# Kernel optimization log

Measured on AMD Instinct MI355X. Metric: run time of the kernel, lower is better.

The kernel has to match this reference:

```python
import jax, jax.numpy as jnp
import numpy as np

Z, H, M, N, Y = 128, 512, 256, 10, 4   # z_size, hidden, mem_vec, mem_size, y_dim
B, T = 2048, 32
SHIFT_IND = np.concatenate([np.roll(np.arange(N), s) for s in (-1, 0, 1)])  # [3*N]


def setup_inputs() -> dict:
    key = jax.random.key(0)
    ks = iter(jax.random.split(key, 48))
    def nrm(shape, s=0.05):
        return jax.random.normal(next(ks), shape, dtype=jnp.float32) * s
    d = {}
    d["z_seq"] = jax.random.normal(next(ks), (B, T, Z), dtype=jnp.float32)
    d["W_ih"] = nrm((4 * H, Z + M)); d["W_hh"] = nrm((4 * H, H))
    d["b_ih"] = jnp.zeros((4 * H,), jnp.float32); d["b_hh"] = jnp.zeros((4 * H,), jnp.float32)
    heads = {"read_key": M, "write_key": M, "erase": M, "add": M, "y": Y,
             "rks": 1, "wks": 1, "rig": 1, "wig": 1, "rsh": 3, "wsh": 3, "rshp": 1, "wshp": 1}
    for nm, o in heads.items():
        d["W_" + nm] = nrm((o, H)); d["b_" + nm] = jnp.zeros((o,), jnp.float32)
    d["memory_init"] = nrm((N, M))
    d["gamma"] = jnp.ones((Z,), jnp.float32)
    d["beta"] = jnp.zeros((Z,), jnp.float32)
    return d


def reference(z_seq, W_ih, W_hh, b_ih, b_hh,
              W_read_key, b_read_key, W_write_key, b_write_key,
              W_erase, b_erase, W_add, b_add, W_y, b_y,
              W_rks, b_rks, W_wks, b_wks, W_rig, b_rig, W_wig, b_wig,
              W_rsh, b_rsh, W_wsh, b_wsh, W_rshp, b_rshp, W_wshp, b_wshp,
              memory_init, gamma, beta):
    Bs, Ts = z_seq.shape[0], z_seq.shape[1]
    eps = 1e-8
    # context norm over the time axis (single task segment), unbiased var as torch
    mu = z_seq.mean(1, keepdims=True)
    sig = jnp.sqrt(z_seq.var(1, ddof=1, keepdims=True) + eps)
    z = (z_seq - mu) / sig * gamma + beta
    z_ext = jnp.concatenate([z, jnp.zeros((Bs, 1, Z), z.dtype)], axis=1)  # t == T step uses zero input
    shift_ind = jnp.asarray(SHIFT_IND)

    def lin(h, W, b):
        return h @ W.T + b

    def cos_sim(key_v, mem):  # key [B,M], mem [B,N,M] -> [B,N]
        dot = jnp.einsum('bm,bnm->bn', key_v, mem)
        kn = jnp.maximum(jnp.linalg.norm(key_v, axis=1, keepdims=True), eps)
        mn = jnp.maximum(jnp.linalg.norm(mem, axis=2), eps)
        return dot / (kn * mn)

    def address(key_v, strength, gate, shift_w, sharpen, w_prev, mem, use_interp):
        # content addressing (exp(s*sim)/sum == softmax), interpolation, circular shift, sharpening
        w = jax.nn.softmax(strength * cos_sim(key_v, mem), axis=1)      # [B,N]
        w = jnp.where(use_interp, gate * w + (1.0 - gate) * w_prev, w)
        w_sh = w[:, shift_ind].reshape(Bs, 3, N)                        # gather per shift
        w = jnp.einsum('bsn,bs->bn', w_sh, shift_w)
        wp = w ** sharpen
        return wp / wp.sum(1, keepdims=True)

    def step(carry, xs):
        h, c, read_vec, mem, w_read, w_write = carry
        z_t, t = xs
        lstm_in = jnp.concatenate([z_t, read_vec], axis=1)              # [B, Z+M]
        gates = lstm_in @ W_ih.T + b_ih + h @ W_hh.T + b_hh
        i, f, g, o = jnp.split(gates, 4, axis=1)
        c = jax.nn.sigmoid(f) * c + jax.nn.sigmoid(i) * jnp.tanh(g)
        h = jax.nn.sigmoid(o) * jnp.tanh(c)
        read_key = jnp.tanh(lin(h, W_read_key, b_read_key))
        write_key = jnp.tanh(lin(h, W_write_key, b_write_key))
        rks = jax.nn.softplus(lin(h, W_rks, b_rks))
        wks = jax.nn.softplus(lin(h, W_wks, b_wks))
        rig = jax.nn.sigmoid(lin(h, W_rig, b_rig))
        wig = jax.nn.sigmoid(lin(h, W_wig, b_wig))
        rsh = jax.nn.softmax(lin(h, W_rsh, b_rsh), axis=1)
        wsh = jax.nn.softmax(lin(h, W_wsh, b_wsh), axis=1)
        rshp = jax.nn.softplus(lin(h, W_rshp, b_rshp)) + 1.0
        wshp = jax.nn.softplus(lin(h, W_wshp, b_wshp)) + 1.0
        erase = jax.nn.sigmoid(lin(h, W_erase, b_erase))
        add = jnp.tanh(lin(h, W_add, b_add))
        y_lin = lin(h, W_y, b_y)
        # read (skipped at t==0; interpolation only for t>1)
        w_read_new = address(read_key, rks, rig, rsh, rshp, w_read, mem, t > 1)
        read_vec = jnp.where(t == 0, jnp.zeros((Bs, M), z_t.dtype),
                             jnp.einsum('bnm,bn->bm', mem, w_read_new))
        w_read = jnp.where(t == 0, w_read, w_read_new)
        # write (every step; interpolation only for t>0)
        w_write = address(write_key, wks, wig, wsh, wshp, w_write, mem, t > 0)
        ww = w_write[:, :, None]
        mem = mem * (1.0 - erase[:, None, :] * ww) + add[:, None, :] * ww
        return (h, c, read_vec, mem, w_read, w_write), y_lin

    carry0 = (jnp.zeros((Bs, H), z.dtype), jnp.zeros((Bs, H), z.dtype),
              jnp.zeros((Bs, M), z.dtype),
              jnp.broadcast_to(memory_init, (Bs, N, M)).astype(z.dtype),
              jnp.zeros((Bs, N), z.dtype), jnp.zeros((Bs, N), z.dtype))
    ts = jnp.arange(Ts + 1)
    _, ys = jax.lax.scan(step, carry0, (jnp.swapaxes(z_ext, 0, 1), ts))
    y_pred_linear = ys[-1]  # output of the final (t == T) step
    return y_pred_linear, jnp.argmax(y_pred_linear, axis=1)
```

## Files before the change

### kernel.cpp

```cpp
#include <hip/hip_runtime.h>
#include <hip/hip_bf16.h>

typedef __attribute__((ext_vector_type(8))) short short8;
typedef __attribute__((ext_vector_type(4))) float f32x4;

#define Bsz   2048
#define Tsz   32
#define Zsz   128
#define Hsz   512
#define Msz   256
#define Nsz   10
#define KDIM  896
#define NGATE 2048
#define NHEAD 1040
#define NHEADP 1152

#define ACT_S ((size_t)Bsz * 768)
#define ZPL_S ((size_t)33 * Bsz * 128)
#define WG_S  ((size_t)NGATE * KDIM)
#define WH_S  ((size_t)NHEADP * Hsz)

__device__ __forceinline__ float sigmoidf_(float x) { return 1.f / (1.f + expf(-x)); }
__device__ __forceinline__ float softplusf_(float x) { return x > 20.f ? x : log1pf(expf(x)); }

__device__ __forceinline__ void split3(float v, __hip_bfloat16& o1, __hip_bfloat16& o2, __hip_bfloat16& o3) {
    o1 = __float2bfloat16(v);
    float r = v - __bfloat162float(o1);
    o2 = __float2bfloat16(r);
    r -= __bfloat162float(o2);
    o3 = __float2bfloat16(r);
}

#define MFMA16(A, B, C) __builtin_amdgcn_mfma_f32_16x16x32_bf16((A), (B), (C), 0, 0, 0)

__device__ __forceinline__ void gload16(const void* g, void* l) {
    __builtin_amdgcn_global_load_lds(
        (const __attribute__((address_space(1))) void*)g,
        (__attribute__((address_space(3))) void*)l, 16, 0, 0);
}


__global__ __launch_bounds__(256) void k_lnorm(
    const float* __restrict__ z_seq, const float* __restrict__ gamma,
    const float* __restrict__ beta, __hip_bfloat16* __restrict__ zb)
{
    int idx = blockIdx.x * 256 + threadIdx.x;
    if (idx >= Bsz * Zsz) return;
    int b = idx >> 7, zi = idx & 127;
    const float* p = z_seq + (size_t)b * Tsz * Zsz + zi;
    float v[32];
    float s = 0.f;
#pragma unroll
    for (int t = 0; t < Tsz; t++) { v[t] = p[t * Zsz]; s += v[t]; }
    float mu = s * (1.f / 32.f);
    float ss = 0.f;
#pragma unroll
    for (int t = 0; t < Tsz; t++) { float d = v[t] - mu; ss += d * d; }
    float rs = rsqrtf(ss * (1.f / 31.f) + 1e-8f);
    float ga = gamma[zi], be = beta[zi];
#pragma unroll
    for (int t = 0; t <= Tsz; t++) {
        float val = (t < Tsz) ? (v[t] - mu) * rs * ga + be : 0.f;
        __hip_bfloat16 a, bq, c;
        split3(val, a, bq, c);
        size_t o = ((size_t)t * Bsz + b) * 128 + zi;
        zb[o] = a; zb[o + ZPL_S] = bq; zb[o + 2 * ZPL_S] = c;
    }
}

__global__ __launch_bounds__(256) void k_prep_wcat(
    const float* __restrict__ W_ih, const float* __restrict__ W_hh,
    const float* __restrict__ b_ih, const float* __restrict__ b_hh,
    __hip_bfloat16* __restrict__ Wt, float* __restrict__ bcat)
{
    int idx = blockIdx.x * 256 + threadIdx.x;
    if (idx >= NGATE * KDIM) return;
    int n = idx / KDIM, k = idx % KDIM;
    int jl = n & 15, g = (n >> 4) & 3, jg = n >> 6;
    int r = g * Hsz + jg * 16 + jl;
    float v = (k < 384) ? W_ih[(size_t)r * 384 + k] : W_hh[(size_t)r * Hsz + (k - 384)];
    __hip_bfloat16 a, b, c;
    split3(v, a, b, c);
    Wt[idx] = a; Wt[idx + WG_S] = b; Wt[idx + 2 * WG_S] = c;
    if (k == 0) bcat[n] = b_ih[r] + b_hh[r];
}

struct HeadP { const float* W[13]; const float* b[13]; };

__global__ __launch_bounds__(256) void k_prep_heads(
    HeadP hp, __hip_bfloat16* __restrict__ Wt, float* __restrict__ bh)
{
    int idx = blockIdx.x * 256 + threadIdx.x;
    if (idx >= NHEADP * Hsz) return;
    int n = idx / Hsz, k = idx % Hsz;
    float v = 0.f;
    if (n < NHEAD) {
        const int offs[14] = {0,256,512,768,1024,1028,1029,1030,1031,1032,1035,1038,1039,1040};
        int h = 0;
        while (n >= offs[h + 1]) h++;
        int local = n - offs[h];
        v = hp.W[h][(size_t)local * Hsz + k];
        if (k == 0) bh[n] = hp.b[h][local];
    } else if (k == 0) bh[n] = 0.f;
    __hip_bfloat16 a, b, c;
    split3(v, a, b, c);
    Wt[idx] = a; Wt[idx + WH_S] = b; Wt[idx + 2 * WH_S] = c;
}

__global__ __launch_bounds__(256) void k_init(
    __hip_bfloat16* __restrict__ act,
    float* __restrict__ cbuf, float* __restrict__ w_read, float* __restrict__ w_write,
    float* __restrict__ mem, const float* __restrict__ memory_init)
{
    int tid = blockIdx.x * blockDim.x + threadIdx.x;
    int stride = gridDim.x * blockDim.x;
    const __hip_bfloat16 z0 = __float2bfloat16(0.f);
    for (size_t i = tid; i < 6 * ACT_S; i += stride) act[i] = z0;
    for (int i = tid; i < Bsz * Hsz; i += stride) cbuf[i] = 0.f;
    for (int i = tid; i < Bsz * Nsz; i += stride) { w_read[i] = 0.f; w_write[i] = 0.f; }
    for (int i = tid; i < Bsz * Nsz * Msz; i += stride) mem[i] = memory_init[i % (Nsz * Msz)];
}


__device__ __forceinline__ void stage_tile(
    uint8_t* smem, int wid, int lane,
    const __hip_bfloat16* aP0, size_t aPlaneStride, int aRowStride, int aColOff, int row0,
    const __hip_bfloat16* bP0, size_t bPlaneStride, int bRowStride, int n00,
    int k0)
{
    const int row4 = lane >> 2;
    const int sch = (lane & 3) ^ (row4 & 3);
    const int koff = sch << 3;
#pragma unroll
    for (int i = 0; i < 9; ++i) {
        int c = wid * 9 + i;
        if (c < 24) {
            int p = c >> 3, rg = c & 7;
            int row = rg * 16 + row4;
            const __hip_bfloat16* g = aP0 + (size_t)p * aPlaneStride +
                (size_t)(row0 + row) * aRowStride + aColOff + k0 + koff;
            gload16(g, smem + p * 8192 + rg * 1024);
        } else {
            int c2 = c - 24;
            int p = c2 >> 2, rg = c2 & 3;
            int row = rg * 16 + row4;
            const __hip_bfloat16* g = bP0 + (size_t)p * bPlaneStride +
                (size_t)(n00 + row) * bRowStride + k0 + koff;
            gload16(g, smem + 24576 + p * 4096 + rg * 1024);
        }
    }
}

__global__ __launch_bounds__(256, 2) void k_gates(
    const __hip_bfloat16* __restrict__ zt,
    const __hip_bfloat16* __restrict__ actin,
    const __hip_bfloat16* __restrict__ Wg,
    const float* __restrict__ bcat,
    float* __restrict__ cbuf,
    __hip_bfloat16* __restrict__ actout)
{
    __shared__ __align__(1024) uint8_t smem[36864];
    const int tid = threadIdx.x;
    const int wid = tid >> 6, lane = tid & 63;
    const int fr = lane & 15, kg = lane >> 4;
    const int wr = wid >> 1, wc = wid & 1;
    const int wg = blockIdx.x;
    const int xcd = wg & 7, rr = wg >> 3;
    const int bm = (xcd & 1) * 8 + (rr & 7);
    const int bn = (xcd >> 1) * 8 + (rr >> 3);
    const int row0 = bm * 128, n00 = bn * 64;

    f32x4 acc[4][2];
#pragma unroll
    for (int s = 0; s < 4; ++s)
#pragma unroll
        for (int u = 0; u < 2; ++u) acc[s][u] = f32x4{0.f, 0.f, 0.f, 0.f};

    const int swz = (kg ^ (fr & 3)) << 4;
    constexpr int PA[6] = {0, 0, 1, 0, 1, 2};
    constexpr int PB[6] = {0, 1, 0, 2, 1, 0};

    const int NKT = KDIM / 32;
    for (int kt = 0; kt < NKT; ++kt) {
        const int k0 = kt * 32;
        if (k0 < 128)
            stage_tile(smem, wid, lane, zt, ZPL_S, 128, 0, row0, Wg, WG_S, KDIM, n00, k0);
        else
            stage_tile(smem, wid, lane, actin, ACT_S, 768, -128, row0, Wg, WG_S, KDIM, n00, k0);
        __syncthreads();

        short8 af[3][4];
#pragma unroll
        for (int p = 0; p < 3; ++p)
#pragma unroll
            for (int s = 0; s < 4; ++s)
                af[p][s] = *(const short8*)(smem + p * 8192 + (wr * 64 + s * 16 + fr) * 64 + swz);
        short8 bf[3][2];
#pragma unroll
        for (int p = 0; p < 3; ++p)
#pragma unroll
            for (int u = 0; u < 2; ++u)
                bf[p][u] = *(const short8*)(smem + 24576 + p * 4096 + (wc * 32 + u * 16 + fr) * 64 + swz);

#pragma unroll
        for (int pr = 0; pr < 6; ++pr)
#pragma unroll
            for (int s = 0; s < 4; ++s)
#pragma unroll
                for (int u = 0; u < 2; ++u)
                    acc[s][u] = MFMA16(af[PA[pr]][s], bf[PB[pr]][u], acc[s][u]);
        __syncthreads();
    }

    float* G = (float*)smem;
#pragma unroll
    for (int s = 0; s < 4; ++s)
#pragma unroll
        for (int u = 0; u < 2; ++u) {
            int g = wc * 2 + u;
#pragma unroll
            for (int r = 0; r < 4; ++r) {
                int row = wr * 64 + s * 16 + kg * 4 + r;
                G[(g * 128 + row) * 17 + fr] = acc[s][u][r];
            }
        }
    __syncthreads();

#pragma unroll
    for (int i = 0; i < 8; ++i) {
        int p2 = i * 256 + tid;
        int row = p2 >> 4, jl = p2 & 15;
        int m = row0 + row;
        int j = bn * 16 + jl;
        float iv = G[(0 * 128 + row) * 17 + jl] + bcat[n00 +  0 + jl];
        float fv = G[(1 * 128 + row) * 17 + jl] + bcat[n00 + 16 + jl];
        float gv = G[(2 * 128 + row) * 17 + jl] + bcat[n00 + 32 + jl];
        float ov = G[(3 * 128 + row) * 17 + jl] + bcat[n00 + 48 + jl];
        size_t ci = (size_t)m * Hsz + j;
        float co = cbuf[ci];
        float cn = sigmoidf_(fv) * co + sigmoidf_(iv) * tanhf(gv);
        float hn = sigmoidf_(ov) * tanhf(cn);
        cbuf[ci] = cn;
        __hip_bfloat16 h1, h2, h3;
        split3(hn, h1, h2, h3);
        size_t ho = (size_t)m * 768 + 256 + j;
        actout[ho] = h1; actout[ho + ACT_S] = h2; actout[ho + 2 * ACT_S] = h3;
    }
}

__global__ __launch_bounds__(256, 2) void k_heads(
    const __hip_bfloat16* __restrict__ actout,
    const __hip_bfloat16* __restrict__ Wh,
    const float* __restrict__ bh,
    float* __restrict__ headbuf)
{
    __shared__ __align__(1024) uint8_t smem[36864];
    const int tid = threadIdx.x;
    const int wid = tid >> 6, lane = tid & 63;
    const int fr = lane & 15, kg = lane >> 4;
    const int wr = wid >> 1, wc = wid & 1;
    const int bm = blockIdx.x, bn = blockIdx.y;
    const int row0 = bm * 128, n00 = bn * 64;

    f32x4 acc[4][2];
#pragma unroll
    for (int s = 0; s < 4; ++s)
#pragma unroll
        for (int u = 0; u < 2; ++u) acc[s][u] = f32x4{0.f, 0.f, 0.f, 0.f};

    const int swz = (kg ^ (fr & 3)) << 4;
    constexpr int PA[6] = {0, 0, 1, 0, 1, 2};
    constexpr int PB[6] = {0, 1, 0, 2, 1, 0};

    const int NKT = Hsz / 32;
    for (int kt = 0; kt < NKT; ++kt) {
        stage_tile(smem, wid, lane, actout, ACT_S, 768, 256, row0, Wh, WH_S, Hsz, n00, kt * 32);
        __syncthreads();

        short8 af[3][4];
#pragma unroll
        for (int p = 0; p < 3; ++p)
#pragma unroll
            for (int s = 0; s < 4; ++s)
                af[p][s] = *(const short8*)(smem + p * 8192 + (wr * 64 + s * 16 + fr) * 64 + swz);
        short8 bf[3][2];
#pragma unroll
        for (int p = 0; p < 3; ++p)
#pragma unroll
            for (int u = 0; u < 2; ++u)
                bf[p][u] = *(const short8*)(smem + 24576 + p * 4096 + (wc * 32 + u * 16 + fr) * 64 + swz);

#pragma unroll
        for (int pr = 0; pr < 6; ++pr)
#pragma unroll
            for (int s = 0; s < 4; ++s)
#pragma unroll
                for (int u = 0; u < 2; ++u)
                    acc[s][u] = MFMA16(af[PA[pr]][s], bf[PB[pr]][u], acc[s][u]);
        __syncthreads();
    }

#pragma unroll
    for (int s = 0; s < 4; ++s)
#pragma unroll
        for (int u = 0; u < 2; ++u) {
            int n = n00 + wc * 32 + u * 16 + fr;
            if (n >= NHEAD) continue;
            float bias = bh[n];
#pragma unroll
            for (int r = 0; r < 4; ++r) {
                int m = row0 + wr * 64 + s * 16 + kg * 4 + r;
                headbuf[(size_t)m * NHEAD + n] = acc[s][u][r] + bias;
            }
        }
}


__global__ __launch_bounds__(256) void k_dots(
    const float* __restrict__ headbuf,
    const float* __restrict__ mem,
    float* __restrict__ dots)
{
    const int b = blockIdx.x;
    const int tid = threadIdx.x;
    const float* hb = headbuf + (size_t)b * NHEAD;
    const float* memb = mem + (size_t)b * Nsz * Msz;

    __shared__ float P[32][257];

    const float rk = tanhf(hb[tid]);
    const float wk = tanhf(hb[256 + tid]);

#pragma unroll
    for (int n = 0; n < 10; n++) {
        float mv = memb[n * Msz + tid];
        P[n][tid]      = rk * mv;
        P[10 + n][tid] = wk * mv;
        P[20 + n][tid] = mv * mv;
    }
    P[30][tid] = rk * rk;
    P[31][tid] = wk * wk;
    __syncthreads();

    const int s = tid >> 3, c = tid & 7;
    float v = 0.f;
#pragma unroll
    for (int i = 0; i < 32; ++i)
        v += P[s][c * 32 + ((i + 4 * c) & 31)];
    v += __shfl_xor(v, 1, 64);
    v += __shfl_xor(v, 2, 64);
    v += __shfl_xor(v, 4, 64);
    if (c == 0) dots[(size_t)b * 32 + s] = v;
}

__device__ inline void compute_address(
    const float dot[10], const float mn[10], float kn, float strength, float gate,
    const float sh[3], float sharp, const float* __restrict__ wprev, bool interp,
    float out[10])
{
    float w[10];
    float mx = -1e30f;
#pragma unroll
    for (int n = 0; n < 10; n++) {
        w[n] = strength * (dot[n] / (kn * mn[n]));
        mx = fmaxf(mx, w[n]);
    }
    float s = 0.f;
#pragma unroll
    for (int n = 0; n < 10; n++) { w[n] = expf(w[n] - mx); s += w[n]; }
    float inv = 1.f / s;
#pragma unroll
    for (int n = 0; n < 10; n++) w[n] *= inv;
    if (interp) {
#pragma unroll
        for (int n = 0; n < 10; n++) w[n] = gate * w[n] + (1.f - gate) * wprev[n];
    }
    float w2[10];
#pragma unroll
    for (int n = 0; n < 10; n++) {
        int np1 = (n + 1) % 10, nm1 = (n + 9) % 10;
        w2[n] = sh[0] * w[np1] + sh[1] * w[n] + sh[2] * w[nm1];
    }
    float ssum = 0.f;
#pragma unroll
    for (int n = 0; n < 10; n++) { w2[n] = powf(w2[n], sharp); ssum += w2[n]; }
    float rinv = 1.f / ssum;
#pragma unroll
    for (int n = 0; n < 10; n++) out[n] = w2[n] * rinv;
}

__global__ __launch_bounds__(256) void k_upd(
    const float* __restrict__ headbuf,
    const float* __restrict__ dots,
    float* __restrict__ mem,
    float* __restrict__ w_read, float* __restrict__ w_write,
    __hip_bfloat16* __restrict__ actout,
    float* __restrict__ d_out,
    int t)
{
    const int b = blockIdx.x;
    const int tid = threadIdx.x;
    const int wid = tid >> 6, lane = tid & 63;
    const float eps = 1e-8f;
    const float* hb = headbuf + (size_t)b * NHEAD;
    float* memb = mem + (size_t)b * Nsz * Msz;

    __shared__ float W2[20];

    const float er = sigmoidf_(hb[512 + tid]);
    const float ad = tanhf(hb[768 + tid]);
    float mreg[10];
#pragma unroll
    for (int n = 0; n < 10; n++) mreg[n] = memb[n * Msz + tid];

    if (wid == 0) {
        const float* db = dots + (size_t)b * 32;
        float dotr[10], dotw[10], mn[10];
#pragma unroll
        for (int n = 0; n < 10; n++) {
            dotr[n] = db[n];
            dotw[n] = db[10 + n];
            mn[n] = fmaxf(sqrtf(db[20 + n]), eps);
        }
        const float knr = fmaxf(sqrtf(db[30]), eps);
        const float knw = fmaxf(sqrtf(db[31]), eps);

        float rks = softplusf_(hb[1028]);
        float wks = softplusf_(hb[1029]);
        float rig = sigmoidf_(hb[1030]);
        float wig = sigmoidf_(hb[1031]);
        float rsh[3], wsh[3];
        {
            float a0 = hb[1032], a1 = hb[1033], a2 = hb[1034];
            float mx = fmaxf(a0, fmaxf(a1, a2));
            float e0 = expf(a0 - mx), e1 = expf(a1 - mx), e2 = expf(a2 - mx);
            float inv = 1.f / (e0 + e1 + e2);
            rsh[0] = e0 * inv; rsh[1] = e1 * inv; rsh[2] = e2 * inv;
            a0 = hb[1035]; a1 = hb[1036]; a2 = hb[1037];
            mx = fmaxf(a0, fmaxf(a1, a2));
            e0 = expf(a0 - mx); e1 = expf(a1 - mx); e2 = expf(a2 - mx);
            inv = 1.f / (e0 + e1 + e2);
            wsh[0] = e0 * inv; wsh[1] = e1 * inv; wsh[2] = e2 * inv;
        }
        float rshp = softplusf_(hb[1038]) + 1.f;
        float wshp = softplusf_(hb[1039]) + 1.f;

        float wfr[10], wfw[10];
        compute_address(dotr, mn, knr, rks, rig, rsh, rshp, w_read + (size_t)b * Nsz, t > 1, wfr);
        compute_address(dotw, mn, knw, wks, wig, wsh, wshp, w_write + (size_t)b * Nsz, t > 0, wfw);

        if (lane < 10) {
            W2[lane] = wfr[lane];
            W2[10 + lane] = wfw[lane];
            if (t != 0) w_read[(size_t)b * Nsz + lane] = wfr[lane];
            w_write[(size_t)b * Nsz + lane] = wfw[lane];
        }
    }
    __syncthreads();

    {
        float rv = 0.f;
#pragma unroll
        for (int n = 0; n < 10; n++) rv += mreg[n] * W2[n];
        if (t == 0) rv = 0.f;
        __hip_bfloat16 r1, r2, r3;
        split3(rv, r1, r2, r3);
        size_t o = (size_t)b * 768 + tid;
        actout[o] = r1; actout[o + ACT_S] = r2; actout[o + 2 * ACT_S] = r3;
    }
#pragma unroll
    for (int n = 0; n < 10; n++) {
        float wwn = W2[10 + n];
        memb[n * Msz + tid] = mreg[n] * (1.f - er * wwn) + ad * wwn;
    }
    if (t == Tsz) {
        if (tid < 4) d_out[(size_t)b * 4 + tid] = hb[1024 + tid];
        if (tid == 0) {
            float y0 = hb[1024], y1 = hb[1025], y2 = hb[1026], y3 = hb[1027];
            int idx = 0; float best = y0;
            if (y1 > best) { best = y1; idx = 1; }
            if (y2 > best) { best = y2; idx = 2; }
            if (y3 > best) { best = y3; idx = 3; }
            d_out[Bsz * 4 + b] = (float)idx;
        }
    }
}


extern "C" void kernel_launch(void* const* d_in, const int* in_sizes, int n_in,
                              void* d_out, int out_size, void* d_ws, size_t ws_size,
                              hipStream_t stream) {
    const float* z_seq = (const float*)d_in[0];
    const float* W_ih  = (const float*)d_in[1];
    const float* W_hh  = (const float*)d_in[2];
    const float* b_ih  = (const float*)d_in[3];
    const float* b_hh  = (const float*)d_in[4];
    const float* memory_init = (const float*)d_in[31];
    const float* gamma = (const float*)d_in[32];
    const float* beta  = (const float*)d_in[33];

    HeadP hp;
    for (int i = 0; i < 13; i++) {
        hp.W[i] = (const float*)d_in[5 + 2 * i];
        hp.b[i] = (const float*)d_in[6 + 2 * i];
    }

    char* ws = (char*)d_ws;
    size_t off = 0;
    auto alloc = [&](size_t bytes) -> void* {
        off = (off + 255) & ~(size_t)255;
        void* p = ws + off;
        off += bytes;
        return p;
    };
    __hip_bfloat16* zbuf  = (__hip_bfloat16*)alloc(3 * ZPL_S * 2);
    __hip_bfloat16* act   = (__hip_bfloat16*)alloc(2 * 3 * ACT_S * 2);
    float* cbuf    = (float*)alloc((size_t)Bsz * Hsz * 4);
    float* mem     = (float*)alloc((size_t)Bsz * Nsz * Msz * 4);
    float* w_read  = (float*)alloc((size_t)Bsz * Nsz * 4);
    float* w_write = (float*)alloc((size_t)Bsz * Nsz * 4);
    float* headbuf = (float*)alloc((size_t)Bsz * NHEAD * 4);
    float* dots    = (float*)alloc((size_t)Bsz * 32 * 4);
    __hip_bfloat16* Wg = (__hip_bfloat16*)alloc(3 * WG_S * 2);
    float* bcat    = (float*)alloc((size_t)NGATE * 4);
    __hip_bfloat16* Wh = (__hip_bfloat16*)alloc(3 * WH_S * 2);
    float* bhead   = (float*)alloc((size_t)NHEADP * 4);

    k_prep_wcat<<<(NGATE * KDIM + 255) / 256, 256, 0, stream>>>(W_ih, W_hh, b_ih, b_hh, Wg, bcat);
    k_prep_heads<<<(NHEADP * Hsz + 255) / 256, 256, 0, stream>>>(hp, Wh, bhead);
    k_lnorm<<<(Bsz * Zsz + 255) / 256, 256, 0, stream>>>(z_seq, gamma, beta, zbuf);
    k_init<<<2048, 256, 0, stream>>>(act, cbuf, w_read, w_write, mem, memory_init);

    float* out_f = (float*)d_out;
    for (int t = 0; t <= Tsz; t++) {
        const __hip_bfloat16* ain = act + (size_t)(t & 1) * 3 * ACT_S;
        __hip_bfloat16*       aout = act + (size_t)((t + 1) & 1) * 3 * ACT_S;
        k_gates<<<512, 256, 0, stream>>>(
            zbuf + (size_t)t * Bsz * 128, ain, Wg, bcat, cbuf, aout);
        k_heads<<<dim3(16, 18), 256, 0, stream>>>(aout, Wh, bhead, headbuf);
        k_dots<<<Bsz, 256, 0, stream>>>(headbuf, mem, dots);
        k_upd<<<Bsz, 256, 0, stream>>>(headbuf, dots, mem, w_read, w_write, aout, out_f, t);
    }
}
```

Before: 4.018 ms.

## Fuse dot-product kernel into memory update and trim final-step work

Folds the per-batch cosine-similarity dot reduction into the addressing/update kernel, so the dots buffer round-trip through global memory and one launch per step go away, and memory is read once instead of twice. The final step (t == T) now computes only the head tile containing the y outputs (blocks starting at column 1024) and skips addressing and memory update, writing outputs from a small separate kernel. The trade-off is higher shared-memory use in the fused kernel, which may reduce occupancy.

```diff
diff --git a/kernel.cpp b/kernel.cpp
--- a/kernel.cpp
+++ b/kernel.cpp
@@ -252,14 +252,15 @@
     const __hip_bfloat16* __restrict__ actout,
     const __hip_bfloat16* __restrict__ Wh,
     const float* __restrict__ bh,
-    float* __restrict__ headbuf)
+    float* __restrict__ headbuf,
+    int nOff)
 {
     __shared__ __align__(1024) uint8_t smem[36864];
     const int tid = threadIdx.x;
     const int wid = tid >> 6, lane = tid & 63;
     const int fr = lane & 15, kg = lane >> 4;
     const int wr = wid >> 1, wc = wid & 1;
-    const int bm = blockIdx.x, bn = blockIdx.y;
+    const int bm = blockIdx.x, bn = blockIdx.y + nOff;
     const int row0 = bm * 128, n00 = bn * 64;
 
     f32x4 acc[4][2];
@@ -316,43 +317,6 @@
 }
 
 
-__global__ __launch_bounds__(256) void k_dots(
-    const float* __restrict__ headbuf,
-    const float* __restrict__ mem,
-    float* __restrict__ dots)
-{
-    const int b = blockIdx.x;
-    const int tid = threadIdx.x;
-    const float* hb = headbuf + (size_t)b * NHEAD;
-    const float* memb = mem + (size_t)b * Nsz * Msz;
-
-    __shared__ float P[32][257];
-
-    const float rk = tanhf(hb[tid]);
-    const float wk = tanhf(hb[256 + tid]);
-
-#pragma unroll
-    for (int n = 0; n < 10; n++) {
-        float mv = memb[n * Msz + tid];
-        P[n][tid]      = rk * mv;
-        P[10 + n][tid] = wk * mv;
-        P[20 + n][tid] = mv * mv;
-    }
-    P[30][tid] = rk * rk;
-    P[31][tid] = wk * wk;
-    __syncthreads();
-
-    const int s = tid >> 3, c = tid & 7;
-    float v = 0.f;
-#pragma unroll
-    for (int i = 0; i < 32; ++i)
-        v += P[s][c * 32 + ((i + 4 * c) & 31)];
-    v += __shfl_xor(v, 1, 64);
-    v += __shfl_xor(v, 2, 64);
-    v += __shfl_xor(v, 4, 64);
-    if (c == 0) dots[(size_t)b * 32 + s] = v;
-}
-
 __device__ inline void compute_address(
     const float dot[10], const float mn[10], float kn, float strength, float gate,
     const float sh[3], float sharp, const float* __restrict__ wprev, bool interp,
@@ -389,13 +353,11 @@
     for (int n = 0; n < 10; n++) out[n] = w2[n] * rinv;
 }
 
-__global__ __launch_bounds__(256) void k_upd(
+__global__ __launch_bounds__(256) void k_addr2(
     const float* __restrict__ headbuf,
-    const float* __restrict__ dots,
     float* __restrict__ mem,
     float* __restrict__ w_read, float* __restrict__ w_write,
     __hip_bfloat16* __restrict__ actout,
-    float* __restrict__ d_out,
     int t)
 {
     const int b = blockIdx.x;
@@ -405,25 +367,51 @@
     const float* hb = headbuf + (size_t)b * NHEAD;
     float* memb = mem + (size_t)b * Nsz * Msz;
 
+    __shared__ float P[32][257];
+    __shared__ float fin[32];
     __shared__ float W2[20];
 
+    const float rk = tanhf(hb[tid]);
+    const float wk = tanhf(hb[256 + tid]);
     const float er = sigmoidf_(hb[512 + tid]);
     const float ad = tanhf(hb[768 + tid]);
+
     float mreg[10];
 #pragma unroll
-    for (int n = 0; n < 10; n++) mreg[n] = memb[n * Msz + tid];
+    for (int n = 0; n < 10; n++) {
+        float mv = memb[n * Msz + tid];
+        mreg[n] = mv;
+        P[n][tid]      = rk * mv;
+        P[10 + n][tid] = wk * mv;
+        P[20 + n][tid] = mv * mv;
+    }
+    P[30][tid] = rk * rk;
+    P[31][tid] = wk * wk;
+    __syncthreads();
+
+    {
+        const int s = tid >> 3, c = tid & 7;
+        float v = 0.f;
+#pragma unroll
+        for (int i = 0; i < 32; ++i)
+            v += P[s][c * 32 + ((i + 4 * c) & 31)];
+        v += __shfl_xor(v, 1, 64);
+        v += __shfl_xor(v, 2, 64);
+        v += __shfl_xor(v, 4, 64);
+        if (c == 0) fin[s] = v;
+    }
+    __syncthreads();
 
     if (wid == 0) {
-        const float* db = dots + (size_t)b * 32;
         float dotr[10], dotw[10], mn[10];
 #pragma unroll
         for (int n = 0; n < 10; n++) {
-            dotr[n] = db[n];
-            dotw[n] = db[10 + n];
-            mn[n] = fmaxf(sqrtf(db[20 + n]), eps);
+            dotr[n] = fin[n];
+            dotw[n] = fin[10 + n];
+            mn[n] = fmaxf(sqrtf(fin[20 + n]), eps);
         }
-        const float knr = fmaxf(sqrtf(db[30]), eps);
-        const float knw = fmaxf(sqrtf(db[31]), eps);
+        const float knr = fmaxf(sqrtf(fin[30]), eps);
+        const float knw = fmaxf(sqrtf(fin[31]), eps);
 
         float rks = softplusf_(hb[1028]);
         float wks = softplusf_(hb[1029]);
@@ -473,17 +461,23 @@
         float wwn = W2[10 + n];
         memb[n * Msz + tid] = mreg[n] * (1.f - er * wwn) + ad * wwn;
     }
-    if (t == Tsz) {
-        if (tid < 4) d_out[(size_t)b * 4 + tid] = hb[1024 + tid];
-        if (tid == 0) {
-            float y0 = hb[1024], y1 = hb[1025], y2 = hb[1026], y3 = hb[1027];
-            int idx = 0; float best = y0;
-            if (y1 > best) { best = y1; idx = 1; }
-            if (y2 > best) { best = y2; idx = 2; }
-            if (y3 > best) { best = y3; idx = 3; }
-            d_out[Bsz * 4 + b] = (float)idx;
-        }
-    }
+}
+
+__global__ __launch_bounds__(64) void k_out(
+    const float* __restrict__ headbuf, float* __restrict__ d_out)
+{
+    int b = blockIdx.x * 64 + threadIdx.x;
+    if (b >= Bsz) return;
+    float4 y = *reinterpret_cast<const float4*>(headbuf + (size_t)b * NHEAD + 1024);
+    d_out[(size_t)b * 4 + 0] = y.x;
+    d_out[(size_t)b * 4 + 1] = y.y;
+    d_out[(size_t)b * 4 + 2] = y.z;
+    d_out[(size_t)b * 4 + 3] = y.w;
+    int idx = 0; float best = y.x;
+    if (y.y > best) { best = y.y; idx = 1; }
+    if (y.z > best) { best = y.z; idx = 2; }
+    if (y.w > best) { best = y.w; idx = 3; }
+    d_out[Bsz * 4 + b] = (float)idx;
 }
 
 
@@ -520,7 +514,6 @@
     float* w_read  = (float*)alloc((size_t)Bsz * Nsz * 4);
     float* w_write = (float*)alloc((size_t)Bsz * Nsz * 4);
     float* headbuf = (float*)alloc((size_t)Bsz * NHEAD * 4);
-    float* dots    = (float*)alloc((size_t)Bsz * 32 * 4);
     __hip_bfloat16* Wg = (__hip_bfloat16*)alloc(3 * WG_S * 2);
     float* bcat    = (float*)alloc((size_t)NGATE * 4);
     __hip_bfloat16* Wh = (__hip_bfloat16*)alloc(3 * WH_S * 2);
@@ -532,13 +525,21 @@
     k_init<<<2048, 256, 0, stream>>>(act, cbuf, w_read, w_write, mem, memory_init);
 
     float* out_f = (float*)d_out;
-    for (int t = 0; t <= Tsz; t++) {
+    for (int t = 0; t < Tsz; t++) {
         const __hip_bfloat16* ain = act + (size_t)(t & 1) * 3 * ACT_S;
         __hip_bfloat16*       aout = act + (size_t)((t + 1) & 1) * 3 * ACT_S;
         k_gates<<<512, 256, 0, stream>>>(
             zbuf + (size_t)t * Bsz * 128, ain, Wg, bcat, cbuf, aout);
-        k_heads<<<dim3(16, 18), 256, 0, stream>>>(aout, Wh, bhead, headbuf);
-        k_dots<<<Bsz, 256, 0, stream>>>(headbuf, mem, dots);
-        k_upd<<<Bsz, 256, 0, stream>>>(headbuf, dots, mem, w_read, w_write, aout, out_f, t);
-    }
-}
+        k_heads<<<dim3(16, 18), 256, 0, stream>>>(aout, Wh, bhead, headbuf, 0);
+        k_addr2<<<Bsz, 256, 0, stream>>>(headbuf, mem, w_read, w_write, aout, t);
+    }
+    {
+        const int t = Tsz;
+        const __hip_bfloat16* ain = act + (size_t)(t & 1) * 3 * ACT_S;
+        __hip_bfloat16*       aout = act + (size_t)((t + 1) & 1) * 3 * ACT_S;
+        k_gates<<<512, 256, 0, stream>>>(
+            zbuf + (size_t)t * Bsz * 128, ain, Wg, bcat, cbuf, aout);
+        k_heads<<<dim3(16, 1), 256, 0, stream>>>(aout, Wh, bhead, headbuf, 16);
+        k_out<<<Bsz / 64, 64, 0, stream>>>(headbuf, out_f);
+    }
+}
```

Measured after the change: 3.862 ms (median of 3 runs). 3.9% less time.
